# Kernel tuning notes

Measured on AMD Instinct MI355X. Metric: run time of the kernel, lower is better.

Reference implementation:

```python
import jax, jax.numpy as jnp
import numpy as np

RADIUS = 0.2
MAX_SAMPLES = 32  # max_samples_per_query


def ball_query(coords, queries, radius, k):
    """coords: [B,Np,3], queries: [B,Nq,3] -> idxs: [B,Nq,k] (first-k in index order,
    empty slots filled with the first valid index, or 0 if no neighbor -- matches
    the standard PointNet++ CUDA ball_query semantics)."""
    Np = coords.shape[1]
    # squared distances [B, Nq, Np]
    diff = queries[:, :, None, :] - coords[:, None, :, :]
    d2 = jnp.sum(diff * diff, axis=-1)
    mask = d2 < radius * radius
    # keys: point index if in-ball else sentinel Np; smallest k keys = first k valid indices
    keys = jnp.where(mask, jnp.arange(Np, dtype=jnp.int32), Np)
    neg_top, _ = jax.lax.top_k(-keys, k)           # largest of -keys == smallest keys
    sorted_keys = -neg_top                          # [B, Nq, k], ascending
    valid = sorted_keys < Np
    first = jnp.where(valid[..., 0:1], sorted_keys[..., 0:1], 0)
    return jnp.where(valid, sorted_keys, first)


def setup_inputs() -> dict:
    key = jax.random.key(0)
    k1, k2, k3, k4 = jax.random.split(key, 4)
    B, Np, Nq, C, Ct = 4, 8192, 2048, 64, 64
    return {
        "points_coords": jax.random.uniform(k1, (B, Np, 3), dtype=jnp.float32),
        "points_features": jax.random.normal(k2, (B, C, Np), dtype=jnp.float32),
        "points_t_embed": jax.random.normal(k3, (B, Ct, Np), dtype=jnp.float32),
        "queries": jax.random.uniform(k4, (B, Nq, 3), dtype=jnp.float32),
    }


def reference(points_coords, points_features, points_t_embed, queries):
    B, Np, _ = points_coords.shape
    Nq = queries.shape[1]
    K = MAX_SAMPLES
    idxs = ball_query(points_coords, queries, RADIUS, K)          # [B,Nq,K] int32
    flat = idxs.reshape(B, Nq * K)
    # grouped coords: gather along point dim then center on queries -> [B,Nq,K,3]
    grouped_coords = jnp.take_along_axis(points_coords, flat[:, :, None], axis=1)
    grouped_coords = grouped_coords.reshape(B, Nq, K, 3) - queries[:, :, None, :]
    # grouped features: gather channel-first along point dim -> [B,C,Nq,K]
    C = points_features.shape[1]
    grouped_features = jnp.take_along_axis(points_features, flat[:, None, :], axis=2)
    grouped_features = grouped_features.reshape(B, C, Nq, K)
    # use_coords=True: prepend centered coords as channels
    grouped_features = jnp.concatenate(
        [grouped_coords.transpose(0, 3, 1, 2), grouped_features], axis=1)  # [B,3+C,Nq,K]
    # t_embed gather -> [B,Ct,Nq,K]
    Ct = points_t_embed.shape[1]
    t_embed = jnp.take_along_axis(points_t_embed, flat[:, None, :], axis=2)
    t_embed = t_embed.reshape(B, Ct, Nq, K)
    return grouped_features, t_embed
```

## Files before the change

### kernel.cpp

```cpp
#include <hip/hip_runtime.h>

constexpr int kB  = 4;
constexpr int kNp = 8192;
constexpr int kNq = 2048;
constexpr int kC  = 64;
constexpr int kCt = 64;
constexpr int kK  = 32;
constexpr float kR2 = (float)(0.2 * 0.2);

__global__ __launch_bounds__(256) void ball_query_kernel(
    const float* __restrict__ coords,
    const float* __restrict__ queries,
    int* __restrict__ idxs)
{
    const int wave = (int)((blockIdx.x * blockDim.x + threadIdx.x) >> 6);
    const int lane = threadIdx.x & 63;
    const int w    = threadIdx.x >> 6;
    const int b    = wave >> 11;
    const int q    = wave & (kNq - 1);

    const float qx = queries[(b * kNq + q) * 3 + 0];
    const float qy = queries[(b * kNq + q) * 3 + 1];
    const float qz = queries[(b * kNq + q) * 3 + 2];

    __shared__ int s_idx[4][kK];

    const float* cb = coords + (size_t)b * kNp * 3;
    int cnt = 0;
    for (int base = 0; base < kNp; base += 64) {
        const int p = base + lane;
        const float cx = cb[p * 3 + 0];
        const float cy = cb[p * 3 + 1];
        const float cz = cb[p * 3 + 2];
        const float dx = __fsub_rn(qx, cx);
        const float dy = __fsub_rn(qy, cy);
        const float dz = __fsub_rn(qz, cz);
        const float d2 = __fadd_rn(__fadd_rn(__fmul_rn(dx, dx), __fmul_rn(dy, dy)),
                                   __fmul_rn(dz, dz));
        const bool in_ball = d2 < kR2;
        const unsigned long long m = __ballot(in_ball);
        if (m) {
            if (in_ball) {
                const int slot = cnt + __popcll(m & ((1ull << lane) - 1ull));
                if (slot < kK) s_idx[w][slot] = p;
            }
            cnt += __popcll(m);
            if (cnt >= kK) break;
        }
    }

    __syncthreads();

    if (lane < kK) {
        int v;
        if (cnt == 0)       v = 0;
        else if (lane < cnt) v = s_idx[w][lane];
        else                 v = s_idx[w][0];
        idxs[(size_t)wave * kK + lane] = v;
    }
}

__global__ __launch_bounds__(256) void transpose_kernel(
    const float* __restrict__ feat,
    const float* __restrict__ temb,
    float* __restrict__ pt)
{
    __shared__ float tile[64][65];

    const int blk = blockIdx.x;
    const int src = blk & 1;
    const int pb  = (blk >> 1) & 127;
    const int b   = blk >> 8;

    const float* in = (src ? temb : feat) + (size_t)b * 64 * kNp + pb * 64;

    {
        const int pl = threadIdx.x & 63;
        const int c0 = threadIdx.x >> 6;
        for (int i = 0; i < 16; ++i) {
            const int ch = c0 + i * 4;
            tile[ch][pl] = in[(size_t)ch * kNp + pl];
        }
    }
    __syncthreads();
    {
        const int ch = threadIdx.x & 63;
        const int p0 = threadIdx.x >> 6;
        float* out = pt + ((size_t)b * kNp + (size_t)pb * 64) * 128 + src * 64;
        for (int i = 0; i < 16; ++i) {
            const int p = p0 + i * 4;
            out[(size_t)p * 128 + ch] = tile[ch][p];
        }
    }
}

__global__ __launch_bounds__(256) void gather_kernel(
    const float* __restrict__ coords,
    const float* __restrict__ queries,
    const int*   __restrict__ idxs,
    const float* __restrict__ pt,
    float* __restrict__ out)
{
    const int bq = blockIdx.x;
    const int b  = bq >> 11;
    const int q  = bq & (kNq - 1);

    __shared__ int   s_idx[kK];
    __shared__ float tile[kK][129];

    if (threadIdx.x < kK) s_idx[threadIdx.x] = idxs[(size_t)bq * kK + threadIdx.x];
    __syncthreads();

    {
        const int ch = threadIdx.x & 127;
        const int kk = threadIdx.x >> 7;
        for (int i = 0; i < 16; ++i) {
            const int k = i * 2 + kk;
            tile[k][ch] = pt[((size_t)b * kNp + s_idx[k]) * 128 + ch];
        }
    }
    __syncthreads();

    float* gf = out + ((size_t)b * 67 * kNq + q) * kK;
    const float* qp = queries + ((size_t)b * kNq + q) * 3;

    if (threadIdx.x < 96) {
        const int c = threadIdx.x >> 5;
        const int k = threadIdx.x & 31;
        const float v = coords[((size_t)b * kNp + s_idx[k]) * 3 + c] - qp[c];
        gf[(size_t)c * kNq * kK + k] = v;
    }
    {
        const int k  = threadIdx.x & 31;
        const int c0 = threadIdx.x >> 5;
        for (int i = 0; i < 8; ++i) {
            const int c = c0 + i * 8;
            gf[(size_t)(3 + c) * kNq * kK + k] = tile[k][c];
        }
    }
    {
        float* te = out + (size_t)kB * 67 * kNq * kK + ((size_t)b * 64 * kNq + q) * kK;
        const int k  = threadIdx.x & 31;
        const int c0 = threadIdx.x >> 5;
        for (int i = 0; i < 8; ++i) {
            const int c = c0 + i * 8;
            te[(size_t)c * kNq * kK + k] = tile[k][64 + c];
        }
    }
}

extern "C" void kernel_launch(void* const* d_in, const int* in_sizes, int n_in,
                              void* d_out, int out_size, void* d_ws, size_t ws_size,
                              hipStream_t stream) {
    const float* coords  = (const float*)d_in[0];
    const float* feats   = (const float*)d_in[1];
    const float* temb    = (const float*)d_in[2];
    const float* queries = (const float*)d_in[3];

    int*   idxs = (int*)d_ws;
    float* pt   = (float*)((char*)d_ws + (size_t)kB * kNq * kK * 4);

    ball_query_kernel<<<kB * kNq / 4, 256, 0, stream>>>(coords, queries, idxs);
    transpose_kernel<<<kB * (kNp / 64) * 2, 256, 0, stream>>>(feats, temb, pt);
    gather_kernel<<<kB * kNq, 256, 0, stream>>>(coords, queries, idxs, pt,
                                                (float*)d_out);
}
```

Baseline: 203.7 us.

## Restructure gather as per-channel LDS row lookup and SoA coords for ball query

Drops the point-major transpose of features and time embeddings. The gather now loads each full channel row (8192 floats) into LDS per block and writes every output index for that channel with coalesced float4 stores. Coordinates are converted to SoA for coalesced ball-query loads, the ball-query loop is unrolled by four with the early-exit check per 256 points, and the centered-coordinate output is written directly from the ball-query kernel. The risks are low occupancy from the 32KB LDS row per block with only 512 blocks, and LDS bank conflicts on the random row lookups.

```diff
diff --git a/kernel.cpp b/kernel.cpp
--- a/kernel.cpp
+++ b/kernel.cpp
@@ -3,15 +3,29 @@
 constexpr int kB  = 4;
 constexpr int kNp = 8192;
 constexpr int kNq = 2048;
-constexpr int kC  = 64;
-constexpr int kCt = 64;
 constexpr int kK  = 32;
 constexpr float kR2 = (float)(0.2 * 0.2);
 
+__global__ __launch_bounds__(256) void coords_soa_kernel(
+    const float* __restrict__ coords, float* __restrict__ cb3)
+{
+    const int t = blockIdx.x * 256 + threadIdx.x;
+    const int b = t >> 13;
+    const int p = t & (kNp - 1);
+    const float x = coords[(size_t)t * 3 + 0];
+    const float y = coords[(size_t)t * 3 + 1];
+    const float z = coords[(size_t)t * 3 + 2];
+    float* o = cb3 + (size_t)b * 3 * kNp;
+    o[0 * kNp + p] = x;
+    o[1 * kNp + p] = y;
+    o[2 * kNp + p] = z;
+}
+
 __global__ __launch_bounds__(256) void ball_query_kernel(
-    const float* __restrict__ coords,
+    const float* __restrict__ cb3,
     const float* __restrict__ queries,
-    int* __restrict__ idxs)
+    int* __restrict__ idxs,
+    float* __restrict__ out)
 {
     const int wave = (int)((blockIdx.x * blockDim.x + threadIdx.x) >> 6);
     const int lane = threadIdx.x & 63;
@@ -23,129 +37,96 @@
     const float qy = queries[(b * kNq + q) * 3 + 1];
     const float qz = queries[(b * kNq + q) * 3 + 2];
 
+    const float* __restrict__ cbx = cb3 + (size_t)b * 3 * kNp;
+    const float* __restrict__ cby = cbx + kNp;
+    const float* __restrict__ cbz = cby + kNp;
+
     __shared__ int s_idx[4][kK];
 
-    const float* cb = coords + (size_t)b * kNp * 3;
+    const unsigned long long lt = (1ull << lane) - 1ull;
     int cnt = 0;
-    for (int base = 0; base < kNp; base += 64) {
-        const int p = base + lane;
-        const float cx = cb[p * 3 + 0];
-        const float cy = cb[p * 3 + 1];
-        const float cz = cb[p * 3 + 2];
-        const float dx = __fsub_rn(qx, cx);
-        const float dy = __fsub_rn(qy, cy);
-        const float dz = __fsub_rn(qz, cz);
-        const float d2 = __fadd_rn(__fadd_rn(__fmul_rn(dx, dx), __fmul_rn(dy, dy)),
-                                   __fmul_rn(dz, dz));
-        const bool in_ball = d2 < kR2;
-        const unsigned long long m = __ballot(in_ball);
-        if (m) {
+    for (int base = 0; base < kNp; base += 256) {
+#pragma unroll
+        for (int j = 0; j < 4; ++j) {
+            const int p = base + j * 64 + lane;
+            const float cx = cbx[p];
+            const float cy = cby[p];
+            const float cz = cbz[p];
+            const float dx = __fsub_rn(qx, cx);
+            const float dy = __fsub_rn(qy, cy);
+            const float dz = __fsub_rn(qz, cz);
+            const float d2 = __fadd_rn(
+                __fadd_rn(__fmul_rn(dx, dx), __fmul_rn(dy, dy)),
+                __fmul_rn(dz, dz));
+            const bool in_ball = d2 < kR2;
+            const unsigned long long m = __ballot(in_ball);
             if (in_ball) {
-                const int slot = cnt + __popcll(m & ((1ull << lane) - 1ull));
+                const int slot = cnt + __popcll(m & lt);
                 if (slot < kK) s_idx[w][slot] = p;
             }
             cnt += __popcll(m);
-            if (cnt >= kK) break;
         }
+        if (cnt >= kK) break;
     }
-
-    __syncthreads();
 
     if (lane < kK) {
         int v;
-        if (cnt == 0)       v = 0;
+        if (cnt == 0)        v = 0;
         else if (lane < cnt) v = s_idx[w][lane];
         else                 v = s_idx[w][0];
         idxs[(size_t)wave * kK + lane] = v;
-    }
-}
 
-__global__ __launch_bounds__(256) void transpose_kernel(
-    const float* __restrict__ feat,
-    const float* __restrict__ temb,
-    float* __restrict__ pt)
-{
-    __shared__ float tile[64][65];
-
-    const int blk = blockIdx.x;
-    const int src = blk & 1;
-    const int pb  = (blk >> 1) & 127;
-    const int b   = blk >> 8;
-
-    const float* in = (src ? temb : feat) + (size_t)b * 64 * kNp + pb * 64;
-
-    {
-        const int pl = threadIdx.x & 63;
-        const int c0 = threadIdx.x >> 6;
-        for (int i = 0; i < 16; ++i) {
-            const int ch = c0 + i * 4;
-            tile[ch][pl] = in[(size_t)ch * kNp + pl];
-        }
-    }
-    __syncthreads();
-    {
-        const int ch = threadIdx.x & 63;
-        const int p0 = threadIdx.x >> 6;
-        float* out = pt + ((size_t)b * kNp + (size_t)pb * 64) * 128 + src * 64;
-        for (int i = 0; i < 16; ++i) {
-            const int p = p0 + i * 4;
-            out[(size_t)p * 128 + ch] = tile[ch][p];
-        }
+        const int k = lane;
+        float* gf = out + ((size_t)(b * 67) * kNq + q) * kK + k;
+        gf[(size_t)0 * kNq * kK] = __fsub_rn(cbx[v], qx);
+        gf[(size_t)1 * kNq * kK] = __fsub_rn(cby[v], qy);
+        gf[(size_t)2 * kNq * kK] = __fsub_rn(cbz[v], qz);
     }
 }
 
 __global__ __launch_bounds__(256) void gather_kernel(
-    const float* __restrict__ coords,
-    const float* __restrict__ queries,
+    const float* __restrict__ feat,
+    const float* __restrict__ temb,
     const int*   __restrict__ idxs,
-    const float* __restrict__ pt,
     float* __restrict__ out)
 {
-    const int bq = blockIdx.x;
-    const int b  = bq >> 11;
-    const int q  = bq & (kNq - 1);
+    const int blk = blockIdx.x;
+    const int b   = blk >> 7;
+    const int j   = blk & 127;
 
-    __shared__ int   s_idx[kK];
-    __shared__ float tile[kK][129];
+    const float* src;
+    float* dst;
+    if (j < 64) {
+        src = feat + ((size_t)b * 64 + j) * kNp;
+        dst = out + (size_t)(b * 67 + 3 + j) * (kNq * kK);
+    } else {
+        src = temb + ((size_t)b * 64 + (j - 64)) * kNp;
+        dst = out + (size_t)kB * 67 * kNq * kK
+                  + (size_t)(b * 64 + (j - 64)) * (kNq * kK);
+    }
 
-    if (threadIdx.x < kK) s_idx[threadIdx.x] = idxs[(size_t)bq * kK + threadIdx.x];
-    __syncthreads();
-
+    __shared__ float row[kNp];
     {
-        const int ch = threadIdx.x & 127;
-        const int kk = threadIdx.x >> 7;
-        for (int i = 0; i < 16; ++i) {
-            const int k = i * 2 + kk;
-            tile[k][ch] = pt[((size_t)b * kNp + s_idx[k]) * 128 + ch];
-        }
+        const float4* s4 = (const float4*)src;
+        float4* r4 = (float4*)row;
+#pragma unroll
+        for (int i = 0; i < kNp / 4 / 256; ++i)
+            r4[i * 256 + threadIdx.x] = s4[i * 256 + threadIdx.x];
     }
     __syncthreads();
 
-    float* gf = out + ((size_t)b * 67 * kNq + q) * kK;
-    const float* qp = queries + ((size_t)b * kNq + q) * 3;
-
-    if (threadIdx.x < 96) {
-        const int c = threadIdx.x >> 5;
-        const int k = threadIdx.x & 31;
-        const float v = coords[((size_t)b * kNp + s_idx[k]) * 3 + c] - qp[c];
-        gf[(size_t)c * kNq * kK + k] = v;
-    }
-    {
-        const int k  = threadIdx.x & 31;
-        const int c0 = threadIdx.x >> 5;
-        for (int i = 0; i < 8; ++i) {
-            const int c = c0 + i * 8;
-            gf[(size_t)(3 + c) * kNq * kK + k] = tile[k][c];
-        }
-    }
-    {
-        float* te = out + (size_t)kB * 67 * kNq * kK + ((size_t)b * 64 * kNq + q) * kK;
-        const int k  = threadIdx.x & 31;
-        const int c0 = threadIdx.x >> 5;
-        for (int i = 0; i < 8; ++i) {
-            const int c = c0 + i * 8;
-            te[(size_t)c * kNq * kK + k] = tile[k][64 + c];
-        }
+    const int4* id4 = (const int4*)(idxs + (size_t)b * kNq * kK);
+    float4* d4 = (float4*)dst;
+    constexpr int total4 = kNq * kK / 4;
+#pragma unroll 4
+    for (int e = threadIdx.x; e < total4; e += 256) {
+        const int4 id = id4[e];
+        float4 v;
+        v.x = row[id.x];
+        v.y = row[id.y];
+        v.z = row[id.z];
+        v.w = row[id.w];
+        d4[e] = v;
     }
 }
 
@@ -156,12 +137,12 @@
     const float* feats   = (const float*)d_in[1];
     const float* temb    = (const float*)d_in[2];
     const float* queries = (const float*)d_in[3];
+    float* out = (float*)d_out;
 
     int*   idxs = (int*)d_ws;
-    float* pt   = (float*)((char*)d_ws + (size_t)kB * kNq * kK * 4);
+    float* cb3  = (float*)((char*)d_ws + (size_t)kB * kNq * kK * 4);
 
-    ball_query_kernel<<<kB * kNq / 4, 256, 0, stream>>>(coords, queries, idxs);
-    transpose_kernel<<<kB * (kNp / 64) * 2, 256, 0, stream>>>(feats, temb, pt);
-    gather_kernel<<<kB * kNq, 256, 0, stream>>>(coords, queries, idxs, pt,
-                                                (float*)d_out);
+    coords_soa_kernel<<<kB * kNp / 256, 256, 0, stream>>>(coords, cb3);
+    ball_query_kernel<<<kB * kNq / 4, 256, 0, stream>>>(cb3, queries, idxs, out);
+    gather_kernel<<<kB * 128, 256, 0, stream>>>(feats, temb, idxs, out);
 }
```

New measurement: 185.2 us. -9.1%, faster.
